# Kernel tuning notes

Hardware: AMD Instinct MI355X
Metric: run time of the kernel (lower is better)

## Reference

```python
import jax, jax.numpy as jnp
import numpy as np

BETA = 0.25
N_E = 8192
E_DIM = 64
B, L = 32, 512


def setup_inputs() -> dict:
    key = jax.random.key(0)
    k1, k2, k3 = jax.random.split(key, 3)
    z = jax.random.normal(k1, (B, E_DIM, L), dtype=jnp.float32)
    mask = jax.random.randint(k2, (B, L), 0, 2, dtype=jnp.int32)
    # nn.Embedding init: uniform(-1/n_e, 1/n_e)
    emb = jax.random.uniform(k3, (N_E, E_DIM), dtype=jnp.float32,
                             minval=-1.0 / N_E, maxval=1.0 / N_E)
    return {"z": z, "mask": mask, "emb": emb}


def reference(z, mask, emb):
    sg = jax.lax.stop_gradient
    b, c, l = z.shape            # c == e_dim
    n_e = emb.shape[0]
    zt = jnp.transpose(z, (0, 2, 1))          # (B, L, C)
    zf = zt.reshape(-1, c)                    # (B*L, C)
    m = mask.reshape(-1, 1).astype(zf.dtype)  # (B*L, 1) per-token mask

    # pairwise squared distances (with masked z, as in original)
    zm = zf * m
    d = (jnp.sum(zf * zf * m, axis=1, keepdims=True)
         + jnp.sum(emb * emb, axis=1)
         - 2.0 * jnp.matmul(zm, emb.T))       # (B*L, n_e)

    idx = jnp.argmin(d, axis=1)               # (B*L,)
    min_encodings = jax.nn.one_hot(idx, n_e, dtype=zf.dtype)  # (B*L, n_e)
    z_q = emb[idx].reshape(zt.shape)          # gather == one_hot @ emb

    # masked MSE losses (mask broadcast over the C dim, mean over mask.sum()*C)
    m3 = m.reshape(b, l, 1)
    denom = jnp.sum(m3) * c
    embedding_loss = jnp.sum((sg(z_q) - zt) ** 2 * m3) / denom
    commitment_loss = jnp.sum((z_q - sg(zt)) ** 2 * m3) / denom
    loss = embedding_loss + BETA * commitment_loss

    # straight-through estimator
    z_q_st = zt + sg(z_q - zt)

    e_mean = jnp.mean(min_encodings, axis=0)
    perplexity = jnp.exp(-jnp.sum(e_mean * jnp.log(e_mean + 1e-10)))

    z_q_out = jnp.transpose(z_q_st, (0, 2, 1))  # back to (B, C, L)
    return loss, z_q_out, perplexity, min_encodings, idx[:, None]
```

## Files before the change

kernel.cpp:

```cpp
#include <hip/hip_runtime.h>
#include <cstdint>
#include <cstddef>

#define TOK 16384
#define NE  8192
#define NTILE 32
#define WWIN 1.5e-4f

#define O_ZQ   1
#define O_PERP 1048577
#define O_ENC  1048578
#define O_IDX  135266306

typedef short bf16x8 __attribute__((ext_vector_type(8)));
typedef float f32x4  __attribute__((ext_vector_type(4)));

__device__ __forceinline__ unsigned short f2bf(float v) {
  unsigned int u = __float_as_uint(v);
  return (unsigned short)((u + 0x7FFFu + ((u >> 16) & 1u)) >> 16);
}

__global__ void k_zero(unsigned long long* se_min) {
  if (threadIdx.x == 0) *se_min = ~0ull;
}

__global__ __launch_bounds__(256) void k_init(
    const float* __restrict__ z, const int* __restrict__ mask,
    const float* __restrict__ emb,
    unsigned long long* __restrict__ packed,
    float* __restrict__ s_z, float* __restrict__ s_e,
    int* __restrict__ hist, float* __restrict__ zt,
    unsigned long long* __restrict__ se_min) {
  int g = blockIdx.x * 256 + threadIdx.x;
  if (g < TOK) {
    int t = g, b = t >> 9, l = t & 511;
    const float* zp = z + (size_t)b * 32768 + l;
    const int mt = mask[t];
    float* ztp = zt + (size_t)t * 64;
    float r[8];
#pragma unroll
    for (int j = 0; j < 8; ++j) {
      float v = mt ? zp[(size_t)j * 512] : 0.0f;
      ztp[j] = v;
      r[j] = __fmul_rn(v, v);
    }
#pragma unroll
    for (int i = 8; i < 64; i += 8)
#pragma unroll
      for (int j = 0; j < 8; ++j) {
        float v = mt ? zp[(size_t)(i + j) * 512] : 0.0f;
        ztp[i + j] = v;
        r[j] = __fadd_rn(r[j], __fmul_rn(v, v));
      }
    float s = __fadd_rn(__fadd_rn(__fadd_rn(r[0], r[1]), __fadd_rn(r[2], r[3])),
                        __fadd_rn(__fadd_rn(r[4], r[5]), __fadd_rn(r[6], r[7])));
    s_z[t] = s;
    packed[t] = ~0ull;
  } else if (g < TOK + NE) {
    int i = g - TOK;
    const float* ep = emb + (size_t)i * 64;
    float r[8];
#pragma unroll
    for (int j = 0; j < 8; ++j) { float v = ep[j]; r[j] = __fmul_rn(v, v); }
#pragma unroll
    for (int kk = 8; kk < 64; kk += 8)
#pragma unroll
      for (int j = 0; j < 8; ++j) { float v = ep[kk + j]; r[j] = __fadd_rn(r[j], __fmul_rn(v, v)); }
    float s = __fadd_rn(__fadd_rn(__fadd_rn(r[0], r[1]), __fadd_rn(r[2], r[3])),
                        __fadd_rn(__fadd_rn(r[4], r[5]), __fadd_rn(r[6], r[7])));
    s_e[i] = s;
    hist[i] = 0;
    unsigned long long p = ((unsigned long long)__float_as_uint(s) << 32) | (unsigned int)i;
    atomicMin(se_min, p);
  }
}

__global__ __launch_bounds__(256, 1) void k_mfma(
    const float* __restrict__ z, const int* __restrict__ mask,
    const float* __restrict__ emb,
    const float* __restrict__ s_z, const float* __restrict__ s_e,
    unsigned int* __restrict__ tilemin, float* __restrict__ enc_out) {
  __shared__ __align__(16) unsigned short zs[128][64];
  __shared__ __align__(16) unsigned short es[256][64];
  __shared__ unsigned int tmins[128];

  const int tid   = threadIdx.x;
  const int tslot = blockIdx.x;
  const int I0    = tslot * 256;
  const int T0    = blockIdx.y * 128;
  const int b     = T0 >> 9;
  const int l0    = T0 & 511;

  {
    const int tok = tid & 127, kh = tid >> 7;
    const int mt  = mask[T0 + tok];
    const float* zp = z + (size_t)b * 32768 + l0 + tok;
#pragma unroll
    for (int i = 0; i < 4; ++i) {
      int k0 = kh * 32 + i * 8;
      float v0 = mt ? zp[(size_t)(k0 + 0) * 512] : 0.0f;
      float v1 = mt ? zp[(size_t)(k0 + 1) * 512] : 0.0f;
      float v2 = mt ? zp[(size_t)(k0 + 2) * 512] : 0.0f;
      float v3 = mt ? zp[(size_t)(k0 + 3) * 512] : 0.0f;
      float v4 = mt ? zp[(size_t)(k0 + 4) * 512] : 0.0f;
      float v5 = mt ? zp[(size_t)(k0 + 5) * 512] : 0.0f;
      float v6 = mt ? zp[(size_t)(k0 + 6) * 512] : 0.0f;
      float v7 = mt ? zp[(size_t)(k0 + 7) * 512] : 0.0f;
      unsigned int w0 = (unsigned int)f2bf(v0) | ((unsigned int)f2bf(v1) << 16);
      unsigned int w1 = (unsigned int)f2bf(v2) | ((unsigned int)f2bf(v3) << 16);
      unsigned int w2 = (unsigned int)f2bf(v4) | ((unsigned int)f2bf(v5) << 16);
      unsigned int w3 = (unsigned int)f2bf(v6) | ((unsigned int)f2bf(v7) << 16);
      int slot = (k0 >> 3) ^ (tok & 7);
      *(uint4*)&zs[tok][slot * 8] = make_uint4(w0, w1, w2, w3);
    }
  }
  {
    const int code_ = tid >> 2, q = tid & 3;
#pragma unroll
    for (int co = 0; co < 4; ++co) {
      int code = co * 64 + code_;
      const float* ep = emb + (size_t)(I0 + code) * 64 + q * 16;
      unsigned int w[8];
#pragma unroll
      for (int j = 0; j < 8; ++j)
        w[j] = (unsigned int)f2bf(ep[2 * j]) | ((unsigned int)f2bf(ep[2 * j + 1]) << 16);
      int s0 = (q * 2) ^ (code & 7), s1 = (q * 2 + 1) ^ (code & 7);
      *(uint4*)&es[code][s0 * 8] = make_uint4(w[0], w[1], w[2], w[3]);
      *(uint4*)&es[code][s1 * 8] = make_uint4(w[4], w[5], w[6], w[7]);
    }
  }
  if (tid < 128) tmins[tid] = 0x7F800000u;
  __syncthreads();

  const int l  = tid & 63, w = tid >> 6;
  const int wr = w >> 1, wc = w & 1;
  const int rA = l & 15;
  const int kg = l >> 4;

  f32x4 acc[4][8];
#pragma unroll
  for (int fr = 0; fr < 4; ++fr)
#pragma unroll
    for (int fc = 0; fc < 8; ++fc)
#pragma unroll
      for (int r = 0; r < 4; ++r) acc[fr][fc][r] = 0.0f;

  float* encb = enc_out + (size_t)T0 * 8192 + I0;

#pragma unroll
  for (int q = 0; q < 2; ++q) {
    bf16x8 af[4], bfv[8];
#pragma unroll
    for (int fr = 0; fr < 4; ++fr) {
      int row  = wr * 64 + fr * 16 + rA;
      int slot = (q * 4 + kg) ^ (row & 7);
      af[fr] = *(const bf16x8*)&zs[row][slot * 8];
    }
#pragma unroll
    for (int fc = 0; fc < 8; ++fc) {
      int crow = wc * 128 + fc * 16 + rA;
      int slot = (q * 4 + kg) ^ (crow & 7);
      bfv[fc] = *(const bf16x8*)&es[crow][slot * 8];
    }
#pragma unroll
    for (int fr = 0; fr < 4; ++fr)
#pragma unroll
      for (int fc = 0; fc < 8; ++fc)
        acc[fr][fc] = __builtin_amdgcn_mfma_f32_16x16x32_bf16(af[fr], bfv[fc], acc[fr][fc], 0, 0, 0);

#pragma unroll
    for (int it = 0; it < 16; ++it) {
      int id  = q * 4096 + it * 256 + tid;
      int row = id >> 6, c4 = id & 63;
      *(float4*)(encb + (size_t)row * 8192 + c4 * 4) = make_float4(0.f, 0.f, 0.f, 0.f);
    }
  }

  float sev[8];
#pragma unroll
  for (int fc = 0; fc < 8; ++fc) sev[fc] = s_e[I0 + wc * 128 + fc * 16 + rA];

#pragma unroll
  for (int fr = 0; fr < 4; ++fr) {
#pragma unroll
    for (int r = 0; r < 4; ++r) {
      int tok = wr * 64 + fr * 16 + kg * 4 + r;
      float szv = s_z[T0 + tok];
      float dm = __uint_as_float(0x7F800000u);
#pragma unroll
      for (int fc = 0; fc < 8; ++fc)
        dm = fminf(dm, (szv + sev[fc]) - 2.0f * acc[fr][fc][r]);
      dm = fminf(dm, __shfl_xor(dm, 1, 64));
      dm = fminf(dm, __shfl_xor(dm, 2, 64));
      dm = fminf(dm, __shfl_xor(dm, 4, 64));
      dm = fminf(dm, __shfl_xor(dm, 8, 64));
      if (rA == 0) atomicMin(&tmins[tok], __float_as_uint(dm));
    }
  }
  __syncthreads();
  if (tid < 128)
    tilemin[(size_t)(T0 + tid) * NTILE + tslot] = tmins[tid];
}

__global__ __launch_bounds__(256) void k_window(
    const int* __restrict__ mask, const unsigned int* __restrict__ tilemin,
    const unsigned long long* __restrict__ se_min,
    unsigned long long* __restrict__ packed, float* __restrict__ thresh) {
  int t = blockIdx.x * 256 + threadIdx.x;
  if (mask[t]) {
    unsigned int mn = 0xFFFFFFFFu;
    const uint4* tm = (const uint4*)(tilemin + (size_t)t * NTILE);
#pragma unroll
    for (int i = 0; i < 8; ++i) {
      uint4 v = tm[i];
      mn = min(mn, min(min(v.x, v.y), min(v.z, v.w)));
    }
    thresh[t] = __uint_as_float(mn) + WWIN;
  } else {
    packed[t] = *se_min;
    thresh[t] = -1.0f;
  }
}

__global__ __launch_bounds__(256, 2) void k_exact(
    const float* __restrict__ zt, const float* __restrict__ emb,
    const float* __restrict__ s_z, const float* __restrict__ s_e,
    const unsigned int* __restrict__ tilemin, const float* __restrict__ thresh,
    unsigned long long* __restrict__ packed) {
  __shared__ __align__(16) float elT[64][260];
  const int tile = blockIdx.x;
  const int C0   = tile * 256;
  const int tid  = threadIdx.x, l = tid & 63, w = tid >> 6;

#pragma unroll
  for (int pass = 0; pass < 16; ++pass) {
    int gid = pass * 256 + tid;
    int code = gid >> 4, kq = gid & 15;
    float4 v = *(const float4*)(emb + (size_t)(C0 + code) * 64 + kq * 4);
    elT[kq * 4 + 0][code] = v.x;
    elT[kq * 4 + 1][code] = v.y;
    elT[kq * 4 + 2][code] = v.z;
    elT[kq * 4 + 3][code] = v.w;
  }
  __syncthreads();

  const int gw   = blockIdx.y * 4 + w;
  const int base = gw * 512;

  for (int s = 0; s < 8; ++s) {
    int tt = base + s * 64 + l;
    float th = thresh[tt];
    unsigned int tm = tilemin[(size_t)tt * NTILE + tile];
    unsigned long long bal = __ballot(__uint_as_float(tm) <= th);
    while (bal) {
      int bit = __ffsll((long long)bal) - 1;
      bal &= bal - 1;
      int t = base + s * 64 + bit;
      const float* zr = zt + (size_t)t * 64;
      float szt = s_z[t];
      float a0 = 0.f, a1 = 0.f, a2 = 0.f, a3 = 0.f;
#pragma unroll 8
      for (int k = 0; k < 64; ++k) {
        float zk = zr[k];
        float4 e4 = *(const float4*)&elT[k][4 * l];
        a0 = fmaf(e4.x, zk, a0);
        a1 = fmaf(e4.y, zk, a1);
        a2 = fmaf(e4.z, zk, a2);
        a3 = fmaf(e4.w, zk, a3);
      }
      unsigned long long best = ~0ull;
      float av[4] = {a0, a1, a2, a3};
#pragma unroll
      for (int q = 0; q < 4; ++q) {
        int code = C0 + 4 * l + q;
        float d = __fsub_rn(__fadd_rn(szt, s_e[code]), __fmul_rn(2.0f, av[q]));
        unsigned int db = __float_as_uint(d);
        db = ((int)db < 0) ? ~db : (db | 0x80000000u);
        unsigned long long p = ((unsigned long long)db << 32) | (unsigned int)code;
        best = (p < best) ? p : best;
      }
#pragma unroll
      for (int off = 1; off < 64; off <<= 1) {
        unsigned long long q = __shfl_xor(best, off, 64);
        best = (q < best) ? q : best;
      }
      if (l == 0) atomicMin(&packed[t], best);
    }
  }
}

__global__ __launch_bounds__(512) void k_finalize(
    const float* __restrict__ z, const int* __restrict__ mask,
    const float* __restrict__ emb,
    const unsigned long long* __restrict__ packed,
    float* __restrict__ out_zq, float* __restrict__ out_enc,
    float* __restrict__ out_idx,
    int* __restrict__ hist, float* __restrict__ token_loss) {
  __shared__ float part[8][64];
  const int T0   = blockIdx.x * 64;
  const int lane = threadIdx.x & 63;
  const int w    = threadIdx.x >> 6;
  const int b    = T0 >> 9;
  const int l0   = T0 & 511;
  const int t    = T0 + lane;

  const int idx = (int)(unsigned int)(packed[t] & 0xFFFFFFFFu);

  const float* zb = z      + (size_t)b * 32768 + l0 + lane;
  float*       qb = out_zq + (size_t)b * 32768 + l0 + lane;

  float sq = 0.0f;
#pragma unroll
  for (int cc = 0; cc < 8; ++cc) {
    int c = w * 8 + cc;
    float zv   = zb[(size_t)c * 512];
    float e    = emb[(size_t)idx * 64 + c];
    float diff = __fsub_rn(e, zv);
    qb[(size_t)c * 512] = __fadd_rn(zv, diff);
    sq = fmaf(diff, diff, sq);
  }
  part[w][lane] = sq;
  __syncthreads();

  if (w == 0) {
    float s = __fadd_rn(
        __fadd_rn(__fadd_rn(part[0][lane], part[1][lane]),
                  __fadd_rn(part[2][lane], part[3][lane])),
        __fadd_rn(__fadd_rn(part[4][lane], part[5][lane]),
                  __fadd_rn(part[6][lane], part[7][lane])));
    token_loss[t] = mask[t] ? s : 0.0f;
    out_idx[t] = (float)idx;
    out_enc[(size_t)t * 8192 + idx] = 1.0f;
    atomicAdd(&hist[idx], 1);
  }
}

__global__ __launch_bounds__(256) void k_partial(
    const float* __restrict__ token_loss, const int* __restrict__ mask,
    const int* __restrict__ hist, float* __restrict__ partials) {
  __shared__ float sf[256], sm[256], sh[256];
  const int bb = blockIdx.x, tid = threadIdx.x;
  int ti = bb * 256 + tid;
  sf[tid] = token_loss[ti];
  sm[tid] = (float)mask[ti];
  float h = 0.f;
  if (tid < 128) {
    float pm = (float)hist[bb * 128 + tid] * (1.0f / 16384.0f);
    h = pm * logf(pm + 1e-10f);
  }
  sh[tid] = h;
  __syncthreads();
  for (int off = 128; off; off >>= 1) {
    if (tid < off) { sf[tid] += sf[tid + off]; sm[tid] += sm[tid + off]; sh[tid] += sh[tid + off]; }
    __syncthreads();
  }
  if (tid == 0) {
    partials[bb]       = sf[0];
    partials[64 + bb]  = sm[0];
    partials[128 + bb] = sh[0];
  }
}

__global__ __launch_bounds__(64) void k_final(
    const float* __restrict__ partials, float* __restrict__ out) {
  int tn = threadIdx.x;
  float lo = partials[tn], mc = partials[64 + tn], en = partials[128 + tn];
#pragma unroll
  for (int off = 32; off; off >>= 1) {
    lo += __shfl_down(lo, off, 64);
    mc += __shfl_down(mc, off, 64);
    en += __shfl_down(en, off, 64);
  }
  if (tn == 0) {
    float denom = mc * 64.0f;
    float el = lo / denom;
    out[0]      = __fadd_rn(el, __fmul_rn(0.25f, el));
    out[O_PERP] = expf(-en);
  }
}

extern "C" void kernel_launch(void* const* d_in, const int* in_sizes, int n_in,
                              void* d_out, int out_size, void* d_ws, size_t ws_size,
                              hipStream_t stream) {
  const float* z    = (const float*)d_in[0];
  const int*   mask = (const int*)d_in[1];
  const float* emb  = (const float*)d_in[2];
  float* out = (float*)d_out;
  char*  ws  = (char*)d_ws;

  unsigned long long* packed  = (unsigned long long*)ws;
  float*              s_z     = (float*)(ws + 131072);
  float*              s_e     = (float*)(ws + 196608);
  int*                hist    = (int*)(ws + 229376);
  float*              token_loss = (float*)(ws + 262144);
  float*              partials   = (float*)(ws + 327680);
  unsigned long long* se_min  = (unsigned long long*)(ws + 331776);
  float*              thresh  = (float*)(ws + 335872);
  unsigned int*       tilemin = (unsigned int*)(ws + 401408);
  float*              zt      = (float*)(ws + 2498560);

  k_zero<<<1, 64, 0, stream>>>(se_min);
  k_init<<<96, 256, 0, stream>>>(z, mask, emb, packed, s_z, s_e, hist, zt, se_min);

  dim3 gm(32, 128, 1);
  k_mfma<<<gm, 256, 0, stream>>>(z, mask, emb, s_z, s_e, tilemin, out + O_ENC);

  k_window<<<64, 256, 0, stream>>>(mask, tilemin, se_min, packed, thresh);

  dim3 ge(32, 8, 1);
  k_exact<<<ge, 256, 0, stream>>>(zt, emb, s_z, s_e, tilemin, thresh, packed);

  k_finalize<<<256, 512, 0, stream>>>(z, mask, emb, packed,
                                      out + O_ZQ, out + O_ENC, out + O_IDX,
                                      hist, token_loss);

  k_partial<<<64, 256, 0, stream>>>(token_loss, mask, hist, partials);
  k_final<<<1, 64, 0, stream>>>(partials, out);
}
```

Before: 363.1 us.

## Transpose zt and tilemin to column-major and merge final reductions into one kernel

```diff
diff --git a/kernel.cpp b/kernel.cpp
--- a/kernel.cpp
+++ b/kernel.cpp
@@ -36,12 +36,11 @@
     int t = g, b = t >> 9, l = t & 511;
     const float* zp = z + (size_t)b * 32768 + l;
     const int mt = mask[t];
-    float* ztp = zt + (size_t)t * 64;
     float r[8];
 #pragma unroll
     for (int j = 0; j < 8; ++j) {
       float v = mt ? zp[(size_t)j * 512] : 0.0f;
-      ztp[j] = v;
+      zt[(size_t)j * TOK + t] = v;
       r[j] = __fmul_rn(v, v);
     }
 #pragma unroll
@@ -49,7 +48,7 @@
 #pragma unroll
       for (int j = 0; j < 8; ++j) {
         float v = mt ? zp[(size_t)(i + j) * 512] : 0.0f;
-        ztp[i + j] = v;
+        zt[(size_t)(i + j) * TOK + t] = v;
         r[j] = __fadd_rn(r[j], __fmul_rn(v, v));
       }
     float s = __fadd_rn(__fadd_rn(__fadd_rn(r[0], r[1]), __fadd_rn(r[2], r[3])),
@@ -199,7 +198,7 @@
   }
   __syncthreads();
   if (tid < 128)
-    tilemin[(size_t)(T0 + tid) * NTILE + tslot] = tmins[tid];
+    tilemin[(size_t)tslot * TOK + T0 + tid] = tmins[tid];
 }
 
 __global__ __launch_bounds__(256) void k_window(
@@ -209,12 +208,9 @@
   int t = blockIdx.x * 256 + threadIdx.x;
   if (mask[t]) {
     unsigned int mn = 0xFFFFFFFFu;
-    const uint4* tm = (const uint4*)(tilemin + (size_t)t * NTILE);
-#pragma unroll
-    for (int i = 0; i < 8; ++i) {
-      uint4 v = tm[i];
-      mn = min(mn, min(min(v.x, v.y), min(v.z, v.w)));
-    }
+#pragma unroll
+    for (int i = 0; i < NTILE; ++i)
+      mn = min(mn, tilemin[(size_t)i * TOK + t]);
     thresh[t] = __uint_as_float(mn) + WWIN;
   } else {
     packed[t] = *se_min;
@@ -250,18 +246,17 @@
   for (int s = 0; s < 8; ++s) {
     int tt = base + s * 64 + l;
     float th = thresh[tt];
-    unsigned int tm = tilemin[(size_t)tt * NTILE + tile];
+    unsigned int tm = tilemin[(size_t)tile * TOK + tt];
     unsigned long long bal = __ballot(__uint_as_float(tm) <= th);
     while (bal) {
       int bit = __ffsll((long long)bal) - 1;
       bal &= bal - 1;
       int t = base + s * 64 + bit;
-      const float* zr = zt + (size_t)t * 64;
       float szt = s_z[t];
       float a0 = 0.f, a1 = 0.f, a2 = 0.f, a3 = 0.f;
 #pragma unroll 8
       for (int k = 0; k < 64; ++k) {
-        float zk = zr[k];
+        float zk = zt[(size_t)k * TOK + t];
         float4 e4 = *(const float4*)&elT[k][4 * l];
         a0 = fmaf(e4.x, zk, a0);
         a1 = fmaf(e4.y, zk, a1);
@@ -335,47 +330,28 @@
   }
 }
 
-__global__ __launch_bounds__(256) void k_partial(
+__global__ __launch_bounds__(1024) void k_scalars(
     const float* __restrict__ token_loss, const int* __restrict__ mask,
-    const int* __restrict__ hist, float* __restrict__ partials) {
-  __shared__ float sf[256], sm[256], sh[256];
-  const int bb = blockIdx.x, tid = threadIdx.x;
-  int ti = bb * 256 + tid;
-  sf[tid] = token_loss[ti];
-  sm[tid] = (float)mask[ti];
-  float h = 0.f;
-  if (tid < 128) {
-    float pm = (float)hist[bb * 128 + tid] * (1.0f / 16384.0f);
-    h = pm * logf(pm + 1e-10f);
-  }
-  sh[tid] = h;
-  __syncthreads();
-  for (int off = 128; off; off >>= 1) {
+    const int* __restrict__ hist, float* __restrict__ out) {
+  __shared__ float sf[1024], sm[1024], sh[1024];
+  const int tid = threadIdx.x;
+  float s = 0.f, mc = 0.f, h = 0.f;
+  for (int i = tid; i < TOK; i += 1024) { s += token_loss[i]; mc += (float)mask[i]; }
+  for (int i = tid; i < NE; i += 1024) {
+    float pm = (float)hist[i] * (1.0f / 16384.0f);
+    h += pm * logf(pm + 1e-10f);
+  }
+  sf[tid] = s; sm[tid] = mc; sh[tid] = h;
+  __syncthreads();
+  for (int off = 512; off; off >>= 1) {
     if (tid < off) { sf[tid] += sf[tid + off]; sm[tid] += sm[tid + off]; sh[tid] += sh[tid + off]; }
     __syncthreads();
   }
   if (tid == 0) {
-    partials[bb]       = sf[0];
-    partials[64 + bb]  = sm[0];
-    partials[128 + bb] = sh[0];
-  }
-}
-
-__global__ __launch_bounds__(64) void k_final(
-    const float* __restrict__ partials, float* __restrict__ out) {
-  int tn = threadIdx.x;
-  float lo = partials[tn], mc = partials[64 + tn], en = partials[128 + tn];
-#pragma unroll
-  for (int off = 32; off; off >>= 1) {
-    lo += __shfl_down(lo, off, 64);
-    mc += __shfl_down(mc, off, 64);
-    en += __shfl_down(en, off, 64);
-  }
-  if (tn == 0) {
-    float denom = mc * 64.0f;
-    float el = lo / denom;
+    float denom = sm[0] * 64.0f;
+    float el = sf[0] / denom;
     out[0]      = __fadd_rn(el, __fmul_rn(0.25f, el));
-    out[O_PERP] = expf(-en);
+    out[O_PERP] = expf(-sh[0]);
   }
 }
 
@@ -393,7 +369,6 @@
   float*              s_e     = (float*)(ws + 196608);
   int*                hist    = (int*)(ws + 229376);
   float*              token_loss = (float*)(ws + 262144);
-  float*              partials   = (float*)(ws + 327680);
   unsigned long long* se_min  = (unsigned long long*)(ws + 331776);
   float*              thresh  = (float*)(ws + 335872);
   unsigned int*       tilemin = (unsigned int*)(ws + 401408);
@@ -414,6 +389,5 @@
                                       out + O_ZQ, out + O_ENC, out + O_IDX,
                                       hist, token_loss);
 
-  k_partial<<<64, 256, 0, stream>>>(token_loss, mask, hist, partials);
-  k_final<<<1, 64, 0, stream>>>(partials, out);
-}
+  k_scalars<<<1, 1024, 0, stream>>>(token_loss, mask, hist, out);
+}
```

After: 368.1 us. About the same (+1.4%).
